# Kernel optimization log

Hardware: AMD Instinct MI355X
Metric: run time of the kernel (lower is better)

## Reference

```python
import jax, jax.numpy as jnp
import numpy as np

D_MODEL = 1024
NUM_HEADS = 16
HEAD_DIM = D_MODEL // NUM_HEADS
B, S = 4, 2048


def setup_inputs() -> dict:
    key = jax.random.key(0)
    ks = jax.random.split(key, 11)
    scale = 1.0 / np.sqrt(D_MODEL)
    return {
        "query": jax.random.normal(ks[0], (B, S, D_MODEL), dtype=jnp.float32),
        "key": jax.random.normal(ks[1], (B, S, D_MODEL), dtype=jnp.float32),
        "value": jax.random.normal(ks[2], (B, S, D_MODEL), dtype=jnp.float32),
        "Wq": jax.random.normal(ks[3], (D_MODEL, D_MODEL), dtype=jnp.float32) * scale,
        "bq": jnp.zeros((D_MODEL,), dtype=jnp.float32),
        "Wk": jax.random.normal(ks[4], (D_MODEL, D_MODEL), dtype=jnp.float32) * scale,
        "bk": jnp.zeros((D_MODEL,), dtype=jnp.float32),
        "Wv": jax.random.normal(ks[5], (D_MODEL, D_MODEL), dtype=jnp.float32) * scale,
        "bv": jnp.zeros((D_MODEL,), dtype=jnp.float32),
        "Wo": jax.random.normal(ks[6], (D_MODEL, D_MODEL), dtype=jnp.float32) * scale,
        "bo": jnp.zeros((D_MODEL,), dtype=jnp.float32),
    }


def reference(query, key, value, Wq, bq, Wk, bk, Wv, bv, Wo, bo):
    b = query.shape[0]
    # QKV projections, split into heads: [B, H, S, hd]
    Q = (query @ Wq + bq).reshape(b, -1, NUM_HEADS, HEAD_DIM).transpose(0, 2, 1, 3)
    K = (key @ Wk + bk).reshape(b, -1, NUM_HEADS, HEAD_DIM).transpose(0, 2, 1, 3)
    V = (value @ Wv + bv).reshape(b, -1, NUM_HEADS, HEAD_DIM).transpose(0, 2, 1, 3)
    # scaled dot-product attention, full [B, H, S, S] scores (as in original)
    scores = jnp.einsum("bhqd,bhkd->bhqk", Q, K) / jnp.sqrt(
        jnp.asarray(HEAD_DIM, dtype=jnp.float32))
    attn = jax.nn.softmax(scores, axis=-1)
    out = jnp.einsum("bhqk,bhkd->bhqd", attn, V)
    out = out.transpose(0, 2, 1, 3).reshape(b, -1, D_MODEL)
    return out @ Wo + bo
```

## Files before the change

kernel.cpp:

```cpp
#include <hip/hip_runtime.h>
#include <hip/hip_bf16.h>

typedef _Float16 f16;
typedef _Float16 f16x8 __attribute__((ext_vector_type(8)));
typedef _Float16 f16x4 __attribute__((ext_vector_type(4)));
typedef __fp16 h16x2 __attribute__((ext_vector_type(2)));
typedef float f32x4 __attribute__((ext_vector_type(4)));

#define D_MODEL 1024
#define NHEAD 16
#define HD 64
#define BATCH 4
#define SEQ 2048
#define TOK (BATCH * SEQ)

__device__ __forceinline__ void gload_lds16(const void* g, void* l) {
  __builtin_amdgcn_global_load_lds(
      (const __attribute__((address_space(1))) unsigned int*)g,
      (__attribute__((address_space(3))) unsigned int*)l, 16, 0, 0);
}

__device__ __forceinline__ f16x8 fragF16_64(const char* rowptr, int g, int c) {
  union { uint4 u; f16x8 v; } r;
  r.u = *reinterpret_cast<const uint4*>(rowptr + ((g * 16) ^ ((c & 3) << 4)));
  return r.v;
}
__device__ __forceinline__ f16x8 fragF32_128(const char* rowptr, int g, int c) {
  const int s = (c & 7) << 4;
  union { uint4 u; float f[4]; } a, b;
  a.u = *reinterpret_cast<const uint4*>(rowptr + ((g * 32) ^ s));
  b.u = *reinterpret_cast<const uint4*>(rowptr + ((g * 32 + 16) ^ s));
  f16x8 r;
  r[0] = (f16)a.f[0]; r[1] = (f16)a.f[1]; r[2] = (f16)a.f[2]; r[3] = (f16)a.f[3];
  r[4] = (f16)b.f[0]; r[5] = (f16)b.f[1]; r[6] = (f16)b.f[2]; r[7] = (f16)b.f[3];
  return r;
}
__device__ __forceinline__ f16x8 lds_frag(const char* rowptr, int cb0, int s) {
  const uint2 a = *reinterpret_cast<const uint2*>(rowptr + (cb0 ^ s));
  const uint2 b = *reinterpret_cast<const uint2*>(rowptr + ((cb0 + 32) ^ s));
  union { unsigned int u[4]; f16x8 v; } r;
  r.u[0] = a.x; r.u[1] = a.y; r.u[2] = b.x; r.u[3] = b.y;
  return r.v;
}

__global__ __launch_bounds__(256) void cvt2_k(const float* __restrict__ a,
                                              const float* __restrict__ b,
                                              f16* __restrict__ oa,
                                              f16* __restrict__ ob, int n4) {
  int i = blockIdx.x * 256 + threadIdx.x;
  const float* src = blockIdx.y == 0 ? a : b;
  f16* dst = blockIdx.y == 0 ? oa : ob;
  if (i < n4) {
    float4 v = reinterpret_cast<const float4*>(src)[i];
    f16x4 h;
    h[0] = (f16)v.x; h[1] = (f16)v.y; h[2] = (f16)v.z; h[3] = (f16)v.w;
    reinterpret_cast<f16x4*>(dst)[i] = h;
  }
}

__global__ __launch_bounds__(256) void transpose_cvt4_k(
    const float* __restrict__ w0, const float* __restrict__ w1,
    const float* __restrict__ w2, const float* __restrict__ w3,
    f16* __restrict__ t0, f16* __restrict__ t1, f16* __restrict__ t2,
    f16* __restrict__ t3) {
  __shared__ float tile[32][33];
  const float* W = blockIdx.z == 0 ? w0 : blockIdx.z == 1 ? w1 : blockIdx.z == 2 ? w2 : w3;
  f16* Wt = blockIdx.z == 0 ? t0 : blockIdx.z == 1 ? t1 : blockIdx.z == 2 ? t2 : t3;
  int n0 = blockIdx.x * 32, k0 = blockIdx.y * 32;
  int tx = threadIdx.x & 31, ty = threadIdx.x >> 5;
#pragma unroll
  for (int i = 0; i < 32; i += 8)
    tile[ty + i][tx] = W[(size_t)(k0 + ty + i) * D_MODEL + n0 + tx];
  __syncthreads();
#pragma unroll
  for (int i = 0; i < 32; i += 8)
    Wt[(size_t)(n0 + ty + i) * D_MODEL + k0 + tx] = (f16)tile[tx][ty + i];
}

template <bool A_F32, bool B_F32, bool OUT_F32, bool BIAS_ROW>
__device__ __forceinline__ void gemm_body(
    const void* __restrict__ Ap, const void* __restrict__ Bp,
    const float* __restrict__ bias, void* __restrict__ Cout,
    int M, int N, int K, float scale, int btx, int bty) {
  constexpr int ABUF = A_F32 ? 16384 : 8192;
  constexpr int BBUF = B_F32 ? 16384 : 8192;
  constexpr int BUF = ABUF + BBUF;
  constexpr int NA = A_F32 ? 4 : 2;
  constexpr int NB = B_F32 ? 4 : 2;
  __shared__ char smem[2 * BUF];
  const int tid = threadIdx.x;
  const int lane = tid & 63, wid = tid >> 6;
  const int g = lane >> 4, c = lane & 15;
  const int wm = wid >> 1, wn = wid & 1;
  const size_t brow = (size_t)bty * 128, bcol = (size_t)btx * 128;

  f32x4 acc[4][4];
#pragma unroll
  for (int i = 0; i < 4; ++i)
#pragma unroll
    for (int j = 0; j < 4; ++j) acc[i][j] = (f32x4){0.f, 0.f, 0.f, 0.f};

  const char* ga[NA];
  const char* gb[NB];
#pragma unroll
  for (int j = 0; j < NA; ++j) {
    int ch = wid * NA + j;
    if constexpr (A_F32) {
      int row = ch * 8 + (lane >> 3);
      ga[j] = (const char*)Ap + ((size_t)(brow + row) * K) * 4 +
              (((lane & 7) * 16) ^ ((row & 7) << 4));
    } else {
      int row = ch * 16 + (lane >> 2);
      ga[j] = (const char*)Ap + ((size_t)(brow + row) * K) * 2 +
              (((lane & 3) * 16) ^ ((row & 3) << 4));
    }
  }
#pragma unroll
  for (int j = 0; j < NB; ++j) {
    int ch = wid * NB + j;
    if constexpr (B_F32) {
      int row = ch * 8 + (lane >> 3);
      gb[j] = (const char*)Bp + ((size_t)(bcol + row) * K) * 4 +
              (((lane & 7) * 16) ^ ((row & 7) << 4));
    } else {
      int row = ch * 16 + (lane >> 2);
      gb[j] = (const char*)Bp + ((size_t)(bcol + row) * K) * 2 +
              (((lane & 3) * 16) ^ ((row & 3) << 4));
    }
  }
  auto stage = [&](char* buf) {
#pragma unroll
    for (int j = 0; j < NA; ++j) {
      gload_lds16(ga[j], buf + (wid * NA + j) * 1024);
      ga[j] += A_F32 ? 128 : 64;
    }
#pragma unroll
    for (int j = 0; j < NB; ++j) {
      gload_lds16(gb[j], buf + ABUF + (wid * NB + j) * 1024);
      gb[j] += B_F32 ? 128 : 64;
    }
  };

  stage(smem);
  const int nt = K / 32;
  for (int t = 0; t < nt; ++t) {
    char* cur = smem + (size_t)(t & 1) * BUF;
    char* nxt = smem + (size_t)((t + 1) & 1) * BUF;
    asm volatile("s_waitcnt vmcnt(0)" ::: "memory");
    __syncthreads();
    if (t + 1 < nt) stage(nxt);

    f16x8 Af[4], Bf[4];
#pragma unroll
    for (int fm = 0; fm < 4; ++fm) {
      int row = wm * 64 + fm * 16 + c;
      if constexpr (A_F32) Af[fm] = fragF32_128(cur + row * 128, g, c);
      else Af[fm] = fragF16_64(cur + row * 64, g, c);
    }
#pragma unroll
    for (int fn = 0; fn < 4; ++fn) {
      int row = wn * 64 + fn * 16 + c;
      if constexpr (B_F32) Bf[fn] = fragF32_128(cur + ABUF + row * 128, g, c);
      else Bf[fn] = fragF16_64(cur + ABUF + row * 64, g, c);
    }
#pragma unroll
    for (int fm = 0; fm < 4; ++fm)
#pragma unroll
      for (int fn = 0; fn < 4; ++fn)
        acc[fm][fn] = __builtin_amdgcn_mfma_f32_16x16x32_f16(Af[fm], Bf[fn],
                                                             acc[fm][fn], 0, 0, 0);
  }

#pragma unroll
  for (int fn = 0; fn < 4; ++fn) {
    size_t col = bcol + wn * 64 + fn * 16 + c;
    float cbias = BIAS_ROW ? 0.f : bias[col];
#pragma unroll
    for (int fm = 0; fm < 4; ++fm) {
#pragma unroll
      for (int r = 0; r < 4; ++r) {
        size_t row = brow + wm * 64 + fm * 16 + g * 4 + r;
        float v = (acc[fm][fn][r] + (BIAS_ROW ? bias[row] : cbias)) * scale;
        if (OUT_F32)
          ((float*)Cout)[row * (size_t)N + col] = v;
        else
          ((f16*)Cout)[row * (size_t)N + col] = (f16)v;
      }
    }
  }
}

__device__ __forceinline__ void swz_map(int& btx, int& bty) {
  int lin = blockIdx.x + blockIdx.y * 8;
  int xcd = lin & 7, rest = lin >> 3;
  bty = xcd * 8 + (rest & 7);
  btx = rest >> 3;
}

template <bool A_F32, bool B_F32, bool OUT_F32, bool BIAS_ROW, bool SWZ>
__global__ __launch_bounds__(256) void gemm_k(
    const void* __restrict__ Ap, const void* __restrict__ Bp,
    const float* __restrict__ bias, void* __restrict__ Cout,
    int M, int N, int K, float scale) {
  int btx, bty;
  if constexpr (SWZ) swz_map(btx, bty);
  else { btx = blockIdx.x; bty = blockIdx.y; }
  gemm_body<A_F32, B_F32, OUT_F32, BIAS_ROW>(Ap, Bp, bias, Cout, M, N, K, scale,
                                             btx, bty);
}

__global__ __launch_bounds__(256) void qkproj_k(
    const f16* __restrict__ Xq, const f16* __restrict__ Xk,
    const f16* __restrict__ Wqt, const f16* __restrict__ Wkt,
    const float* __restrict__ bq, const float* __restrict__ bk,
    f16* __restrict__ Qp, f16* __restrict__ Kp, float qscale) {
  int btx, bty;
  swz_map(btx, bty);
  const void* Ap = blockIdx.z ? (const void*)Xk : (const void*)Xq;
  const void* Bp = blockIdx.z ? (const void*)Wkt : (const void*)Wqt;
  const float* bias = blockIdx.z ? bk : bq;
  void* Cout = blockIdx.z ? (void*)Kp : (void*)Qp;
  float scale = blockIdx.z ? 1.0f : qscale;
  gemm_body<false, false, false, false>(Ap, Bp, bias, Cout, TOK, D_MODEL,
                                        D_MODEL, scale, btx, bty);
}

__global__ __launch_bounds__(512) void attn_k(const f16* __restrict__ Q,
                                              const f16* __restrict__ Kp,
                                              const f16* __restrict__ Vt,
                                              f16* __restrict__ AO) {
  __shared__ char smem[65536];
  const int tid = threadIdx.x, lane = tid & 63, wid = tid >> 6;
  const int g = lane >> 4, c = lane & 15;
  const int b = blockIdx.x >> 4, h = blockIdx.x & 15;
  const int qt = blockIdx.y;
  const size_t qrow0 = (size_t)b * SEQ + (size_t)qt * 256;
  const int sr = lane >> 3;
  const int sc = (lane & 7) * 16;
  const float NEG_M = -8.65617025f;
  constexpr int NT = SEQ / 64;

#pragma unroll
  for (int j = 0; j < 4; ++j) {
    int ch = wid * 4 + j;
    int row = ch * 8 + sr;
    const char* gq = (const char*)Q + ((qrow0 + row) * D_MODEL + h * HD) * 2 +
                     (sc ^ (sr << 4));
    gload_lds16(gq, smem + ch * 1024);
  }
  asm volatile("s_waitcnt vmcnt(0)" ::: "memory");
  __syncthreads();

  f16x8 Qf[2][2];
#pragma unroll
  for (int fq = 0; fq < 2; ++fq) {
    int row = wid * 32 + fq * 16 + c;
#pragma unroll
    for (int kk = 0; kk < 2; ++kk) {
      union { uint4 u; f16x8 v; } r;
      r.u = *reinterpret_cast<const uint4*>(
          smem + row * 128 + ((kk * 64 + g * 16) ^ ((c & 7) << 4)));
      Qf[fq][kk] = r.v;
    }
  }
  __syncthreads();

  const char* gk;
  const char* gv;
  {
    int row = wid * 8 + sr;
    gk = (const char*)Kp + (((size_t)b * SEQ + row) * D_MODEL + h * HD) * 2 +
         (sc ^ (sr << 4));
    gv = (const char*)Vt + ((size_t)(h * HD + row) * TOK + (size_t)b * SEQ) * 2 +
         (sc ^ (sr << 4));
  }
#pragma unroll
  for (int tt = 0; tt < 3; ++tt) {
    gload_lds16(gk, smem + tt * 8192 + wid * 1024);
    gload_lds16(gv, smem + 32768 + tt * 8192 + wid * 1024);
    gk += (size_t)64 * D_MODEL * 2;
    gv += 64 * 2;
  }

  f16x8 ones_f;
#pragma unroll
  for (int j = 0; j < 8; ++j) ones_f[j] = (c == 0) ? (f16)1.0f : (f16)0.0f;

  f32x4 o[4][2];
#pragma unroll
  for (int i = 0; i < 4; ++i)
#pragma unroll
    for (int j = 0; j < 2; ++j) o[i][j] = (f32x4){0.f, 0.f, 0.f, 0.f};
  f32x4 o_l[2] = {(f32x4){0.f, 0.f, 0.f, 0.f}, (f32x4){0.f, 0.f, 0.f, 0.f}};

  for (int t = 0; t < NT; ++t) {
    if (t < NT - 2)
      asm volatile("s_waitcnt vmcnt(4)" ::: "memory");
    else if (t == NT - 2)
      asm volatile("s_waitcnt vmcnt(2)" ::: "memory");
    else
      asm volatile("s_waitcnt vmcnt(0)" ::: "memory");
    __builtin_amdgcn_s_barrier();
    asm volatile("" ::: "memory");
    if (t + 3 < NT) {
      gload_lds16(gk, smem + ((t + 3) & 3) * 8192 + wid * 1024);
      gload_lds16(gv, smem + 32768 + ((t + 3) & 3) * 8192 + wid * 1024);
      gk += (size_t)64 * D_MODEL * 2;
      gv += 64 * 2;
    }
    const char* Ks = smem + (t & 3) * 8192;
    const char* Vs = smem + 32768 + (t & 3) * 8192;

    f32x4 st[4][2];
#pragma unroll
    for (int i = 0; i < 4; ++i)
#pragma unroll
      for (int j = 0; j < 2; ++j)
        st[i][j] = (f32x4){NEG_M, NEG_M, NEG_M, NEG_M};
#pragma unroll
    for (int kk = 0; kk < 2; ++kk) {
      f16x8 Kf[4];
#pragma unroll
      for (int km = 0; km < 4; ++km) {
        int row = km * 16 + c;
        union { uint4 u; f16x8 v; } r;
        r.u = *reinterpret_cast<const uint4*>(
            Ks + row * 128 + ((kk * 64 + g * 16) ^ ((c & 7) << 4)));
        Kf[km] = r.v;
      }
      __builtin_amdgcn_s_setprio(1);
#pragma unroll
      for (int km = 0; km < 4; ++km)
#pragma unroll
        for (int fq = 0; fq < 2; ++fq)
          st[km][fq] = __builtin_amdgcn_mfma_f32_16x16x32_f16(Kf[km], Qf[fq][kk],
                                                              st[km][fq], 0, 0, 0);
      __builtin_amdgcn_s_setprio(0);
    }

    f16x8 pb[2][2];
#pragma unroll
    for (int fq = 0; fq < 2; ++fq) {
#pragma unroll
      for (int km = 0; km < 4; ++km)
#pragma unroll
        for (int r = 0; r < 4; ++r)
          st[km][fq][r] = __builtin_amdgcn_exp2f(st[km][fq][r]);
#pragma unroll
      for (int k2 = 0; k2 < 2; ++k2) {
        union { h16x2 h2[4]; f16x8 v; } u;
        u.h2[0] = __builtin_amdgcn_cvt_pkrtz(st[2 * k2][fq][0], st[2 * k2][fq][1]);
        u.h2[1] = __builtin_amdgcn_cvt_pkrtz(st[2 * k2][fq][2], st[2 * k2][fq][3]);
        u.h2[2] = __builtin_amdgcn_cvt_pkrtz(st[2 * k2 + 1][fq][0], st[2 * k2 + 1][fq][1]);
        u.h2[3] = __builtin_amdgcn_cvt_pkrtz(st[2 * k2 + 1][fq][2], st[2 * k2 + 1][fq][3]);
        pb[k2][fq] = u.v;
      }
    }

#pragma unroll
    for (int k2 = 0; k2 < 2; ++k2) {
      f16x8 Vf[4];
#pragma unroll
      for (int fhd = 0; fhd < 4; ++fhd) {
        int row = fhd * 16 + c;
        Vf[fhd] = lds_frag(Vs + row * 128, k2 * 64 + g * 8, (row & 7) << 4);
      }
      __builtin_amdgcn_s_setprio(1);
#pragma unroll
      for (int fhd = 0; fhd < 4; ++fhd)
#pragma unroll
        for (int fq = 0; fq < 2; ++fq)
          o[fhd][fq] = __builtin_amdgcn_mfma_f32_16x16x32_f16(Vf[fhd], pb[k2][fq],
                                                              o[fhd][fq], 0, 0, 0);
#pragma unroll
      for (int fq = 0; fq < 2; ++fq)
        o_l[fq] = __builtin_amdgcn_mfma_f32_16x16x32_f16(ones_f, pb[k2][fq],
                                                         o_l[fq], 0, 0, 0);
      __builtin_amdgcn_s_setprio(0);
    }
  }

#pragma unroll
  for (int fq = 0; fq < 2; ++fq) {
    float L = __shfl(o_l[fq][0], c);
    float rl = 1.0f / L;
    size_t token = qrow0 + wid * 32 + fq * 16 + c;
#pragma unroll
    for (int fhd = 0; fhd < 4; ++fhd) {
      f16x4 vv;
#pragma unroll
      for (int r = 0; r < 4; ++r) vv[r] = (f16)(o[fhd][fq][r] * rl);
      *reinterpret_cast<f16x4*>(AO + token * D_MODEL + h * HD + fhd * 16 + g * 4) = vv;
    }
  }
}

extern "C" void kernel_launch(void* const* d_in, const int* in_sizes, int n_in,
                              void* d_out, int out_size, void* d_ws, size_t ws_size,
                              hipStream_t stream) {
  const float* q32 = (const float*)d_in[0];
  const float* k32 = (const float*)d_in[1];
  const float* v32 = (const float*)d_in[2];
  const float* Wq = (const float*)d_in[3];
  const float* bq = (const float*)d_in[4];
  const float* Wk = (const float*)d_in[5];
  const float* bk = (const float*)d_in[6];
  const float* Wv = (const float*)d_in[7];
  const float* bv = (const float*)d_in[8];
  const float* Wo = (const float*)d_in[9];
  const float* bo = (const float*)d_in[10];

  const size_t TOKD = (size_t)TOK * D_MODEL;
  const size_t WD = (size_t)D_MODEL * D_MODEL;
  f16* Xq = (f16*)d_ws;
  f16* Xk = Xq + TOKD;
  f16* Qp = Xk + TOKD;
  f16* Kp = Qp + TOKD;
  f16* Vt = Kp + TOKD;
  f16* AO = Xq;
  f16* Wqt = Vt + TOKD;
  f16* Wkt = Wqt + WD;
  f16* Wvt = Wkt + WD;
  f16* Wot = Wvt + WD;

  int n4 = (int)(TOKD / 4);
  dim3 gc(n4 / 256, 2);
  cvt2_k<<<gc, 256, 0, stream>>>(q32, k32, Xq, Xk, n4);

  dim3 tg(32, 32, 4);
  transpose_cvt4_k<<<tg, 256, 0, stream>>>(Wq, Wk, Wv, Wo, Wqt, Wkt, Wvt, Wot);

  dim3 gqk(8, 64, 2);
  qkproj_k<<<gqk, 256, 0, stream>>>(Xq, Xk, Wqt, Wkt, bq, bk, Qp, Kp,
                                    0.18033688f);
  dim3 gv(TOK / 128, D_MODEL / 128);
  gemm_k<false, true, false, true, false><<<gv, 256, 0, stream>>>(
      Wvt, v32, bv, Vt, D_MODEL, TOK, D_MODEL, 1.0f);

  dim3 ga(BATCH * NHEAD, SEQ / 256);
  attn_k<<<ga, 512, 0, stream>>>(Qp, Kp, Vt, AO);

  dim3 gq(D_MODEL / 128, TOK / 128);
  gemm_k<false, false, true, false, true><<<gq, 256, 0, stream>>>(
      AO, Wot, bo, (float*)d_out, TOK, D_MODEL, D_MODEL, 1.0f);
}
```

Measured before the change: 206.8 us.

## Add four-stage LDS pipelined f16 GEMM for QK and output projections

Introduces a new f16-only GEMM body with a 4-buffer shared-memory ring, prefetching three K-tiles ahead with async global-to-LDS loads and graded vmcnt waits. It uses a single barrier per iteration and raises wave priority around the MFMA block. The QK projection and output projection kernels switch to it, with the goal of hiding global-memory latency better than the previous double-buffered GEMM. It uses 64KB of LDS per block, which may reduce occupancy.

Result: faster. 197.7 us (-4.4%).

```diff
diff --git a/kernel.cpp b/kernel.cpp
--- a/kernel.cpp
+++ b/kernel.cpp
@@ -75,6 +75,111 @@
 #pragma unroll
   for (int i = 0; i < 32; i += 8)
     Wt[(size_t)(n0 + ty + i) * D_MODEL + k0 + tx] = (f16)tile[tx][ty + i];
+}
+
+__device__ __forceinline__ void swz_map(int& btx, int& bty) {
+  int lin = blockIdx.x + blockIdx.y * 8;
+  int xcd = lin & 7, rest = lin >> 3;
+  bty = xcd * 8 + (rest & 7);
+  btx = rest >> 3;
+}
+
+template <bool OUT_F32, bool BIAS_ROW>
+__device__ __forceinline__ void gemm4_body(
+    const f16* __restrict__ Ap, const f16* __restrict__ Bp,
+    const float* __restrict__ bias, void* __restrict__ Cout,
+    int M, int N, int K, float scale, int btx, int bty) {
+  __shared__ char smem[65536];
+  const int tid = threadIdx.x;
+  const int lane = tid & 63, wid = tid >> 6;
+  const int g = lane >> 4, c = lane & 15;
+  const int wm = wid >> 1, wn = wid & 1;
+  const size_t brow = (size_t)bty * 128, bcol = (size_t)btx * 128;
+
+  f32x4 acc[4][4];
+#pragma unroll
+  for (int i = 0; i < 4; ++i)
+#pragma unroll
+    for (int j = 0; j < 4; ++j) acc[i][j] = (f32x4){0.f, 0.f, 0.f, 0.f};
+
+  const char* ga[2];
+  const char* gb[2];
+#pragma unroll
+  for (int j = 0; j < 2; ++j) {
+    int ch = wid * 2 + j;
+    int row = ch * 16 + (lane >> 2);
+    int off = ((lane & 3) * 16) ^ ((row & 3) << 4);
+    ga[j] = (const char*)Ap + ((size_t)(brow + row) * K) * 2 + off;
+    gb[j] = (const char*)Bp + ((size_t)(bcol + row) * K) * 2 + off;
+  }
+  auto stage = [&](int bi) {
+    char* a = smem + bi * 8192;
+    char* b = smem + 32768 + bi * 8192;
+#pragma unroll
+    for (int j = 0; j < 2; ++j) {
+      gload_lds16(ga[j], a + (wid * 2 + j) * 1024);
+      ga[j] += 64;
+    }
+#pragma unroll
+    for (int j = 0; j < 2; ++j) {
+      gload_lds16(gb[j], b + (wid * 2 + j) * 1024);
+      gb[j] += 64;
+    }
+  };
+
+  const int nt = K / 32;
+  stage(0); stage(1); stage(2);
+  for (int t = 0; t < nt; ++t) {
+    if (t < nt - 2)
+      asm volatile("s_waitcnt vmcnt(8)" ::: "memory");
+    else if (t == nt - 2)
+      asm volatile("s_waitcnt vmcnt(4)" ::: "memory");
+    else
+      asm volatile("s_waitcnt vmcnt(0)" ::: "memory");
+    __builtin_amdgcn_s_barrier();
+    asm volatile("" ::: "memory");
+    if (t + 3 < nt) stage((t + 3) & 3);
+
+    const char* As = smem + (size_t)(t & 3) * 8192;
+    const char* Bs = smem + 32768 + (size_t)(t & 3) * 8192;
+    f16x8 Af[4], Bf[4];
+#pragma unroll
+    for (int fm = 0; fm < 4; ++fm) {
+      int row = wm * 64 + fm * 16 + c;
+      Af[fm] = fragF16_64(As + row * 64, g, c);
+    }
+#pragma unroll
+    for (int fn = 0; fn < 4; ++fn) {
+      int row = wn * 64 + fn * 16 + c;
+      Bf[fn] = fragF16_64(Bs + row * 64, g, c);
+    }
+    __builtin_amdgcn_s_setprio(1);
+#pragma unroll
+    for (int fm = 0; fm < 4; ++fm)
+#pragma unroll
+      for (int fn = 0; fn < 4; ++fn)
+        acc[fm][fn] = __builtin_amdgcn_mfma_f32_16x16x32_f16(Af[fm], Bf[fn],
+                                                             acc[fm][fn], 0, 0, 0);
+    __builtin_amdgcn_s_setprio(0);
+  }
+
+#pragma unroll
+  for (int fn = 0; fn < 4; ++fn) {
+    size_t col = bcol + wn * 64 + fn * 16 + c;
+    float cbias = BIAS_ROW ? 0.f : bias[col];
+#pragma unroll
+    for (int fm = 0; fm < 4; ++fm) {
+#pragma unroll
+      for (int r = 0; r < 4; ++r) {
+        size_t row = brow + wm * 64 + fm * 16 + g * 4 + r;
+        float v = (acc[fm][fn][r] + (BIAS_ROW ? bias[row] : cbias)) * scale;
+        if (OUT_F32)
+          ((float*)Cout)[row * (size_t)N + col] = v;
+        else
+          ((f16*)Cout)[row * (size_t)N + col] = (f16)v;
+      }
+    }
+  }
 }
 
 template <bool A_F32, bool B_F32, bool OUT_F32, bool BIAS_ROW>
@@ -190,13 +295,6 @@
   }
 }
 
-__device__ __forceinline__ void swz_map(int& btx, int& bty) {
-  int lin = blockIdx.x + blockIdx.y * 8;
-  int xcd = lin & 7, rest = lin >> 3;
-  bty = xcd * 8 + (rest & 7);
-  btx = rest >> 3;
-}
-
 template <bool A_F32, bool B_F32, bool OUT_F32, bool BIAS_ROW, bool SWZ>
 __global__ __launch_bounds__(256) void gemm_k(
     const void* __restrict__ Ap, const void* __restrict__ Bp,
@@ -209,6 +307,16 @@
                                              btx, bty);
 }
 
+template <bool OUT_F32, bool BIAS_ROW>
+__global__ __launch_bounds__(256) void gemm4_k(
+    const f16* __restrict__ Ap, const f16* __restrict__ Bp,
+    const float* __restrict__ bias, void* __restrict__ Cout,
+    int M, int N, int K, float scale) {
+  int btx, bty;
+  swz_map(btx, bty);
+  gemm4_body<OUT_F32, BIAS_ROW>(Ap, Bp, bias, Cout, M, N, K, scale, btx, bty);
+}
+
 __global__ __launch_bounds__(256) void qkproj_k(
     const f16* __restrict__ Xq, const f16* __restrict__ Xk,
     const f16* __restrict__ Wqt, const f16* __restrict__ Wkt,
@@ -216,13 +324,13 @@
     f16* __restrict__ Qp, f16* __restrict__ Kp, float qscale) {
   int btx, bty;
   swz_map(btx, bty);
-  const void* Ap = blockIdx.z ? (const void*)Xk : (const void*)Xq;
-  const void* Bp = blockIdx.z ? (const void*)Wkt : (const void*)Wqt;
+  const f16* Ap = blockIdx.z ? Xk : Xq;
+  const f16* Bp = blockIdx.z ? Wkt : Wqt;
   const float* bias = blockIdx.z ? bk : bq;
   void* Cout = blockIdx.z ? (void*)Kp : (void*)Qp;
   float scale = blockIdx.z ? 1.0f : qscale;
-  gemm_body<false, false, false, false>(Ap, Bp, bias, Cout, TOK, D_MODEL,
-                                        D_MODEL, scale, btx, bty);
+  gemm4_body<false, false>(Ap, Bp, bias, Cout, TOK, D_MODEL, D_MODEL, scale,
+                           btx, bty);
 }
 
 __global__ __launch_bounds__(512) void attn_k(const f16* __restrict__ Q,
@@ -441,6 +549,6 @@
   attn_k<<<ga, 512, 0, stream>>>(Qp, Kp, Vt, AO);
 
   dim3 gq(D_MODEL / 128, TOK / 128);
-  gemm_k<false, false, true, false, true><<<gq, 256, 0, stream>>>(
+  gemm4_k<true, false><<<gq, 256, 0, stream>>>(
       AO, Wot, bo, (float*)d_out, TOK, D_MODEL, D_MODEL, 1.0f);
 }
```
